# Optimization experiments

Measured on AMD Instinct MI355X. Metric: run time of the kernel, lower is better.

Reference implementation:

```python
import jax, jax.numpy as jnp
import numpy as np

B, T, NX, NY, E, BS = 2, 8, 32, 32, 768, 64
NB = E // BS            # 12 blocks
YM = NY // 2 + 1        # 17 rfft y modes
KM = 12                 # kept_modes (hardcoded in source)
XS = slice(YM - KM, YM + KM)  # slice(5,29) on the x-mode axis (faithful quirk: bounds use y_modes)
LAM = 0.01


def _ln(x, g, b, eps=1e-5):
    m = x.mean(-1, keepdims=True)
    v = ((x - m) ** 2).mean(-1, keepdims=True)
    return (x - m) / jnp.sqrt(v + eps) * g + b


def _softshrink(x, lam=LAM):
    return jnp.where(x > lam, x - lam, jnp.where(x < -lam, x + lam, jnp.zeros((), x.dtype)))


def setup_inputs() -> dict:
    key = jax.random.key(0)
    ks = jax.random.split(key, 8)
    s = 0.02
    return {
        'input': jax.random.normal(ks[0], (B, T, NX * NY, E), jnp.float32),
        'w1': s * jax.random.normal(ks[1], (2, NB, BS, BS), jnp.float32),
        'b1': s * jax.random.normal(ks[2], (2, 1, 1, 1, NB, BS), jnp.float32),
        'w2': s * jax.random.normal(ks[3], (2, NB, BS, BS), jnp.float32),
        'b2': s * jax.random.normal(ks[4], (2, 1, 1, 1, NB, BS), jnp.float32),
        'ln1_g': jnp.ones((E,), jnp.float32),
        'ln1_b': jnp.zeros((E,), jnp.float32),
        'ln2_g': jnp.ones((E,), jnp.float32),
        'ln2_b': jnp.zeros((E,), jnp.float32),
        'mw1': s * jax.random.normal(ks[5], (E, 4 * E), jnp.float32),
        'mb1': jnp.zeros((4 * E,), jnp.float32),
        'mw2': s * jax.random.normal(ks[6], (4 * E, E), jnp.float32),
        'mb2': jnp.zeros((E,), jnp.float32),
    }


def reference(input, w1, b1, w2, b2, ln1_g, ln1_b, ln2_g, ln2_b, mw1, mb1, mw2, mb2):
    residual = input
    h = _ln(input, ln1_g, ln1_b)                       # ln1
    r = h.reshape(B, T, NX, NY, E)
    fc = jnp.fft.rfft2(r, axes=(2, 3), norm='ortho')   # (B,T,NX,YM,E) complex
    fc = fc.reshape(B, T, NX, YM, NB, BS)
    fr = fc.real[:, :, XS, :KM]                        # (B,T,24,12,NB,BS)
    fi = fc.imag[:, :, XS, :KM]
    op = 'btxyni,nio->btxyno'
    o1r = jax.nn.gelu(jnp.einsum(op, fr, w1[0]) - jnp.einsum(op, fi, w1[1]) + b1[0], approximate=False)
    o1i = jax.nn.gelu(jnp.einsum(op, fi, w1[0]) + jnp.einsum(op, fr, w1[1]) + b1[1], approximate=False)
    o2r = jnp.einsum(op, o1r, w2[0]) - jnp.einsum(op, o1i, w2[1]) + b2[0]
    o2i = jnp.einsum(op, o1i, w2[0]) + jnp.einsum(op, o1r, w2[1]) + b2[1]
    out_r = jnp.zeros(fc.shape, jnp.float32).at[:, :, XS, :KM].set(_softshrink(o2r))
    out_i = jnp.zeros(fc.shape, jnp.float32).at[:, :, XS, :KM].set(_softshrink(o2i))
    oc = (out_r + 1j * out_i).reshape(B, T, NX, YM, E)
    spat = jnp.fft.irfft2(oc, s=(NX, NY), axes=(2, 3), norm='ortho').reshape(B, T, NX * NY, E)
    out = spat + h + residual                          # faithful: adds ln1(input) and original input
    res2 = out
    out = _ln(out, ln2_g, ln2_b)                       # ln2
    out = jax.nn.gelu(out @ mw1 + mb1, approximate=False) @ mw2 + mb2
    return out + res2
```

## Files before the change

### kernel.cpp

```cpp
#include <hip/hip_runtime.h>
#include <hip/hip_bf16.h>
#include <math.h>

typedef __bf16 bf16;
typedef __bf16 bf16x8 __attribute__((ext_vector_type(8)));
typedef float f32x4 __attribute__((ext_vector_type(4)));
typedef short short8 __attribute__((ext_vector_type(8)));

#define E_ 768
#define S_ 1024
#define BT_ 16
#define KM_ 12
#define KX_ 24
#define NPOS_ 4608
#define NB_ 12

__device__ __forceinline__ float gelu_exact(float x) {
    return 0.5f * x * (1.0f + erff(x * 0.70710678118654752f));
}

__device__ __forceinline__ bf16x8 neg8(bf16x8 v) {
    short8 s;
    __builtin_memcpy(&s, &v, 16);
    s ^= (short)0x8000;
    bf16x8 r;
    __builtin_memcpy(&r, &s, 16);
    return r;
}

__device__ __forceinline__ void gload16(bf16* lds, const bf16* g) {
    __builtin_amdgcn_global_load_lds(
        (const __attribute__((address_space(1))) void*)g,
        (__attribute__((address_space(3))) void*)lds,
        16, 0, 0);
}

__global__ __launch_bounds__(256) void k_ln_stats(const float* __restrict__ x,
                                                  float* __restrict__ mu, float* __restrict__ rs) {
    int row = blockIdx.x;
    int t = threadIdx.x;
    const float* xr = x + (size_t)row * E_;
    float v0 = xr[t], v1 = xr[t + 256], v2 = xr[t + 512];
    float s = v0 + v1 + v2;
    float ss = v0 * v0 + v1 * v1 + v2 * v2;
    for (int off = 32; off > 0; off >>= 1) {
        s  += __shfl_xor(s, off);
        ss += __shfl_xor(ss, off);
    }
    __shared__ float ls[4], lss[4];
    int w = t >> 6, l = t & 63;
    if (l == 0) { ls[w] = s; lss[w] = ss; }
    __syncthreads();
    if (t == 0) {
        s  = ls[0] + ls[1] + ls[2] + ls[3];
        ss = lss[0] + lss[1] + lss[2] + lss[3];
        float m = s * (1.0f / E_);
        float var = ss * (1.0f / E_) - m * m;
        mu[row] = m;
        rs[row] = rsqrtf(var + 1e-5f);
    }
}

__global__ __launch_bounds__(256) void k_ln2(const float* __restrict__ x,
                                             const float* __restrict__ g,
                                             const float* __restrict__ b,
                                             bf16* __restrict__ out) {
    int row = blockIdx.x;
    int t = threadIdx.x;
    const float* xr = x + (size_t)row * E_;
    float v0 = xr[t], v1 = xr[t + 256], v2 = xr[t + 512];
    float s = v0 + v1 + v2;
    float ss = v0 * v0 + v1 * v1 + v2 * v2;
    for (int off = 32; off > 0; off >>= 1) {
        s  += __shfl_xor(s, off);
        ss += __shfl_xor(ss, off);
    }
    __shared__ float ls[4], lss[4];
    int w = t >> 6, l = t & 63;
    if (l == 0) { ls[w] = s; lss[w] = ss; }
    __syncthreads();
    s  = ls[0] + ls[1] + ls[2] + ls[3];
    ss = lss[0] + lss[1] + lss[2] + lss[3];
    float m = s * (1.0f / E_);
    float var = ss * (1.0f / E_) - m * m;
    float r = rsqrtf(var + 1e-5f);
    #pragma unroll
    for (int q = 0; q < 3; q++) {
        int e = t + q * 256;
        float v = (q == 0) ? v0 : ((q == 1) ? v1 : v2);
        out[(size_t)row * E_ + e] = (bf16)((v - m) * r * g[e] + b[e]);
    }
}

__global__ __launch_bounds__(256) void k_dft_y(const float* __restrict__ inp,
                                               const float* __restrict__ mu, const float* __restrict__ rs,
                                               const float* __restrict__ g, const float* __restrict__ bb,
                                               float* __restrict__ gre, float* __restrict__ gim) {
    int bid = blockIdx.x;
    int ec = bid % 3, x = (bid / 3) % 32, bt = bid / 96;
    int t = threadIdx.x;
    __shared__ float tile[32 * 256];
    __shared__ float c32[32], s32[32];
    if (t < 32) { float a = 6.28318530717958647692f * t / 32.0f; c32[t] = cosf(a); s32[t] = sinf(a); }
    int e = ec * 256 + t;
    float gv = g[e], bv = bb[e];
    int row0 = bt * S_ + x * 32;
    const float* base = inp + (size_t)row0 * E_ + e;
    for (int y = 0; y < 32; y++) {
        float m = mu[row0 + y], r = rs[row0 + y];
        tile[y * 256 + t] = (base[(size_t)y * E_] - m) * r * gv + bv;
    }
    __syncthreads();
    for (int ky = 0; ky < KM_; ky++) {
        float re = 0.f, im = 0.f;
        for (int y = 0; y < 32; y++) {
            int j = (ky * y) & 31;
            float v = tile[y * 256 + t];
            re += v * c32[j];
            im -= v * s32[j];
        }
        size_t o = ((size_t)((bt * 32 + x) * KM_ + ky)) * E_ + e;
        gre[o] = re; gim[o] = im;
    }
}

__global__ __launch_bounds__(256) void k_dft_x(const float* __restrict__ gre, const float* __restrict__ gim,
                                               float* __restrict__ fr, float* __restrict__ fi) {
    int bid = blockIdx.x;
    int ec = bid % 3, ky = (bid / 3) % KM_, bt = bid / (3 * KM_);
    int t = threadIdx.x;
    __shared__ float lre[16 * 256];
    __shared__ float lim[16 * 256];
    __shared__ float c32[32], s32[32];
    if (t < 32) { float a = 6.28318530717958647692f * t / 32.0f; c32[t] = cosf(a); s32[t] = sinf(a); }
    float ar[KX_], ai[KX_];
    #pragma unroll
    for (int k = 0; k < KX_; k++) { ar[k] = 0.f; ai[k] = 0.f; }
    for (int half = 0; half < 2; half++) {
        __syncthreads();
        for (int xi = 0; xi < 16; xi++) {
            int x = half * 16 + xi;
            size_t o = ((size_t)((bt * 32 + x) * KM_ + ky)) * E_ + ec * 256 + t;
            lre[xi * 256 + t] = gre[o];
            lim[xi * 256 + t] = gim[o];
        }
        __syncthreads();
        for (int kxi = 0; kxi < KX_; kxi++) {
            int kx = kxi + 5;
            float re = 0.f, im = 0.f;
            #pragma unroll
            for (int xi = 0; xi < 16; xi++) {
                int j = (kx * (half * 16 + xi)) & 31;
                float c = c32[j], s = s32[j];
                float gr = lre[xi * 256 + t], gi = lim[xi * 256 + t];
                re += gr * c + gi * s;
                im += gi * c - gr * s;
            }
            ar[kxi] += re; ai[kxi] += im;
        }
    }
    #pragma unroll
    for (int kxi = 0; kxi < KX_; kxi++) {
        size_t p = (size_t)(bt * KX_ + kxi) * KM_ + ky;
        fr[p * E_ + ec * 256 + t] = ar[kxi] * (1.0f / 32.0f);
        fi[p * E_ + ec * 256 + t] = ai[kxi] * (1.0f / 32.0f);
    }
}

__global__ __launch_bounds__(256) void k_blockmlp(float* fr, float* fi,
                                                  const float* __restrict__ w1, const float* __restrict__ b1,
                                                  const float* __restrict__ w2, const float* __restrict__ b2) {
    int n = blockIdx.x / 36;
    int p0 = (blockIdx.x % 36) * 128;
    int t = threadIdx.x;
    __shared__ __align__(16) bf16 lXr[128 * 72];
    __shared__ __align__(16) bf16 lXi[128 * 72];
    __shared__ __align__(16) bf16 lW1a[64 * 72];
    __shared__ __align__(16) bf16 lW1b[64 * 72];
    __shared__ __align__(16) bf16 lW2a[64 * 72];
    __shared__ __align__(16) bf16 lW2b[64 * 72];

    {
        int o = t & 63, iq = t >> 6;
        const float* s1a = w1 + (size_t)n * 4096;
        const float* s1b = w1 + (size_t)(NB_ + n) * 4096;
        const float* s2a = w2 + (size_t)n * 4096;
        const float* s2b = w2 + (size_t)(NB_ + n) * 4096;
        #pragma unroll
        for (int ii = 0; ii < 16; ii++) {
            int i = iq * 16 + ii;
            lW1a[o * 72 + i] = (bf16)s1a[i * 64 + o];
            lW1b[o * 72 + i] = (bf16)s1b[i * 64 + o];
            lW2a[o * 72 + i] = (bf16)s2a[i * 64 + o];
            lW2b[o * 72 + i] = (bf16)s2b[i * 64 + o];
        }
    }
    {
        int ch4 = (t & 15) * 4, prow = t >> 4;
        #pragma unroll
        for (int rep = 0; rep < 8; rep++) {
            int p = rep * 16 + prow;
            size_t ga = (size_t)(p0 + p) * E_ + n * 64 + ch4;
            float4 vr = *(const float4*)&fr[ga];
            float4 vi = *(const float4*)&fi[ga];
            bf16 br[4] = {(bf16)vr.x, (bf16)vr.y, (bf16)vr.z, (bf16)vr.w};
            bf16 bi[4] = {(bf16)vi.x, (bf16)vi.y, (bf16)vi.z, (bf16)vi.w};
            *(uint2*)&lXr[p * 72 + ch4] = *(uint2*)br;
            *(uint2*)&lXi[p * 72 + ch4] = *(uint2*)bi;
        }
    }
    int w = t >> 6, l = t & 63, lr = l & 15, lq = l >> 4;
    float bias1r[4], bias1i[4], bias2r[4], bias2i[4];
    #pragma unroll
    for (int ni = 0; ni < 4; ni++) {
        int o = n * 64 + ni * 16 + lr;
        bias1r[ni] = b1[o]; bias1i[ni] = b1[NB_ * 64 + o];
        bias2r[ni] = b2[o]; bias2i[ni] = b2[NB_ * 64 + o];
    }
    __syncthreads();

    f32x4 a1r[2][4], a1i[2][4];
    #pragma unroll
    for (int mt = 0; mt < 2; mt++)
        #pragma unroll
        for (int ni = 0; ni < 4; ni++) { a1r[mt][ni] = (f32x4){0,0,0,0}; a1i[mt][ni] = (f32x4){0,0,0,0}; }
    #pragma unroll
    for (int ks = 0; ks < 2; ks++) {
        int k0 = ks * 32;
        bf16x8 xr[2], xi[2], xin[2];
        #pragma unroll
        for (int mt = 0; mt < 2; mt++) {
            int row = w * 32 + mt * 16 + lr;
            xr[mt]  = *(bf16x8*)&lXr[row * 72 + k0 + lq * 8];
            xi[mt]  = *(bf16x8*)&lXi[row * 72 + k0 + lq * 8];
            xin[mt] = neg8(xi[mt]);
        }
        #pragma unroll
        for (int ni = 0; ni < 4; ni++) {
            bf16x8 ba = *(bf16x8*)&lW1a[(ni * 16 + lr) * 72 + k0 + lq * 8];
            bf16x8 bb = *(bf16x8*)&lW1b[(ni * 16 + lr) * 72 + k0 + lq * 8];
            #pragma unroll
            for (int mt = 0; mt < 2; mt++) {
                a1r[mt][ni] = __builtin_amdgcn_mfma_f32_16x16x32_bf16(xr[mt],  ba, a1r[mt][ni], 0, 0, 0);
                a1r[mt][ni] = __builtin_amdgcn_mfma_f32_16x16x32_bf16(xin[mt], bb, a1r[mt][ni], 0, 0, 0);
                a1i[mt][ni] = __builtin_amdgcn_mfma_f32_16x16x32_bf16(xi[mt],  ba, a1i[mt][ni], 0, 0, 0);
                a1i[mt][ni] = __builtin_amdgcn_mfma_f32_16x16x32_bf16(xr[mt],  bb, a1i[mt][ni], 0, 0, 0);
            }
        }
    }
    #pragma unroll
    for (int mt = 0; mt < 2; mt++)
        #pragma unroll
        for (int ni = 0; ni < 4; ni++) {
            int o = ni * 16 + lr;
            #pragma unroll
            for (int r = 0; r < 4; r++) {
                int row = w * 32 + mt * 16 + lq * 4 + r;
                lXr[row * 72 + o] = (bf16)gelu_exact(a1r[mt][ni][r] + bias1r[ni]);
                lXi[row * 72 + o] = (bf16)gelu_exact(a1i[mt][ni][r] + bias1i[ni]);
            }
        }

    f32x4 a2r[2][4], a2i[2][4];
    #pragma unroll
    for (int mt = 0; mt < 2; mt++)
        #pragma unroll
        for (int ni = 0; ni < 4; ni++) { a2r[mt][ni] = (f32x4){0,0,0,0}; a2i[mt][ni] = (f32x4){0,0,0,0}; }
    #pragma unroll
    for (int ks = 0; ks < 2; ks++) {
        int k0 = ks * 32;
        bf16x8 xr[2], xi[2], xin[2];
        #pragma unroll
        for (int mt = 0; mt < 2; mt++) {
            int row = w * 32 + mt * 16 + lr;
            xr[mt]  = *(bf16x8*)&lXr[row * 72 + k0 + lq * 8];
            xi[mt]  = *(bf16x8*)&lXi[row * 72 + k0 + lq * 8];
            xin[mt] = neg8(xi[mt]);
        }
        #pragma unroll
        for (int ni = 0; ni < 4; ni++) {
            bf16x8 ba = *(bf16x8*)&lW2a[(ni * 16 + lr) * 72 + k0 + lq * 8];
            bf16x8 bb = *(bf16x8*)&lW2b[(ni * 16 + lr) * 72 + k0 + lq * 8];
            #pragma unroll
            for (int mt = 0; mt < 2; mt++) {
                a2r[mt][ni] = __builtin_amdgcn_mfma_f32_16x16x32_bf16(xr[mt],  ba, a2r[mt][ni], 0, 0, 0);
                a2r[mt][ni] = __builtin_amdgcn_mfma_f32_16x16x32_bf16(xin[mt], bb, a2r[mt][ni], 0, 0, 0);
                a2i[mt][ni] = __builtin_amdgcn_mfma_f32_16x16x32_bf16(xi[mt],  ba, a2i[mt][ni], 0, 0, 0);
                a2i[mt][ni] = __builtin_amdgcn_mfma_f32_16x16x32_bf16(xr[mt],  bb, a2i[mt][ni], 0, 0, 0);
            }
        }
    }
    #pragma unroll
    for (int mt = 0; mt < 2; mt++)
        #pragma unroll
        for (int ni = 0; ni < 4; ni++) {
            int o = ni * 16 + lr;
            #pragma unroll
            for (int r = 0; r < 4; r++) {
                int row = w * 32 + mt * 16 + lq * 4 + r;
                float vr = a2r[mt][ni][r] + bias2r[ni];
                float vi = a2i[mt][ni][r] + bias2i[ni];
                vr = (vr > 0.01f) ? vr - 0.01f : ((vr < -0.01f) ? vr + 0.01f : 0.0f);
                vi = (vi > 0.01f) ? vi - 0.01f : ((vi < -0.01f) ? vi + 0.01f : 0.0f);
                size_t ga = (size_t)(p0 + row) * E_ + n * 64 + o;
                fr[ga] = vr;
                fi[ga] = vi;
            }
        }
}

__global__ __launch_bounds__(256) void k_idft_x(const float* __restrict__ pr_, const float* __restrict__ pi_,
                                                float* __restrict__ zre, float* __restrict__ zim) {
    int bid = blockIdx.x;
    int ec = bid % 3, ky = (bid / 3) % KM_, bt = bid / (3 * KM_);
    int t = threadIdx.x;
    __shared__ float lre[KX_ * 256], lim[KX_ * 256];
    __shared__ float c32[32], s32[32];
    if (t < 32) { float a = 6.28318530717958647692f * t / 32.0f; c32[t] = cosf(a); s32[t] = sinf(a); }
    for (int kxi = 0; kxi < KX_; kxi++) {
        size_t p = (size_t)(bt * KX_ + kxi) * KM_ + ky;
        lre[kxi * 256 + t] = pr_[p * E_ + ec * 256 + t];
        lim[kxi * 256 + t] = pi_[p * E_ + ec * 256 + t];
    }
    __syncthreads();
    for (int x = 0; x < 32; x++) {
        float re = 0.f, im = 0.f;
        for (int kxi = 0; kxi < KX_; kxi++) {
            int kx = kxi + 5;
            int j = (kx * x) & 31;
            float c = c32[j], s = s32[j];
            float pr = lre[kxi * 256 + t], pi = lim[kxi * 256 + t];
            re += pr * c - pi * s;
            im += pr * s + pi * c;
        }
        size_t zo = ((size_t)((bt * 32 + x) * KM_ + ky)) * E_ + ec * 256 + t;
        zre[zo] = re; zim[zo] = im;
    }
}

__global__ __launch_bounds__(256) void k_idft_y_res(const float* __restrict__ zre, const float* __restrict__ zim,
                                                    const float* __restrict__ inp,
                                                    const float* __restrict__ mu, const float* __restrict__ rs,
                                                    const float* __restrict__ g, const float* __restrict__ bb,
                                                    float* __restrict__ out) {
    int bid = blockIdx.x;
    int ec = bid % 3, x = (bid / 3) % 32, bt = bid / 96;
    int t = threadIdx.x;
    __shared__ float lre[KM_ * 256], lim[KM_ * 256];
    __shared__ float c32[32], s32[32];
    if (t < 32) { float a = 6.28318530717958647692f * t / 32.0f; c32[t] = cosf(a); s32[t] = sinf(a); }
    for (int ky = 0; ky < KM_; ky++) {
        size_t zo = ((size_t)((bt * 32 + x) * KM_ + ky)) * E_ + ec * 256 + t;
        lre[ky * 256 + t] = zre[zo];
        lim[ky * 256 + t] = zim[zo];
    }
    __syncthreads();
    int e = ec * 256 + t;
    float gv = g[e], bv = bb[e];
    int row0 = bt * S_ + x * 32;
    for (int y = 0; y < 32; y++) {
        float v = lre[t];
        for (int ky = 1; ky < KM_; ky++) {
            int j = (ky * y) & 31;
            v += 2.0f * (lre[ky * 256 + t] * c32[j] - lim[ky * 256 + t] * s32[j]);
        }
        v *= (1.0f / 32.0f);
        size_t o = (size_t)(row0 + y) * E_ + e;
        float iv = inp[o];
        float m = mu[row0 + y], r = rs[row0 + y];
        out[o] = v + ((iv - m) * r * gv + bv) + iv;
    }
}

__global__ void k_transpose_cast(const float* __restrict__ src, bf16* __restrict__ dst, int R, int C) {
    __shared__ float tile[32][33];
    int c0 = blockIdx.x * 32, r0 = blockIdx.y * 32;
    int tx = threadIdx.x, ty = threadIdx.y;
    #pragma unroll
    for (int j = 0; j < 32; j += 8)
        tile[ty + j][tx] = src[(size_t)(r0 + ty + j) * C + c0 + tx];
    __syncthreads();
    #pragma unroll
    for (int j = 0; j < 32; j += 8)
        dst[(size_t)(c0 + ty + j) * R + r0 + tx] = (bf16)tile[tx][ty + j];
}

template<bool FUSE_GELU>
__global__ __launch_bounds__(256) void k_gemm(const bf16* __restrict__ A, const bf16* __restrict__ Bt,
                                              const float* __restrict__ bias, int M, int N, int K,
                                              bf16* __restrict__ outb, float* __restrict__ outf) {
    __shared__ __align__(16) bf16 lA[128 * 32];
    __shared__ __align__(16) bf16 lB[128 * 32];
    int t = threadIdx.x;
    int m0 = blockIdx.x * 128, n0 = blockIdx.y * 128;
    int w = t >> 6, l = t & 63;
    int wm = (w & 1) * 64, wn = (w >> 1) * 64;
    int lr = l & 15, lq = l >> 4;
    f32x4 acc[4][4];
    #pragma unroll
    for (int i = 0; i < 4; i++)
        #pragma unroll
        for (int j = 0; j < 4; j++)
            acc[i][j] = (f32x4){0.f, 0.f, 0.f, 0.f};

    int srow = l >> 2;
    int scol = (l & 3) * 8;
    const bf16* gA0 = A  + (size_t)(m0 + w * 16 + srow) * K + scol;
    const bf16* gA1 = gA0 + (size_t)64 * K;
    const bf16* gB0 = Bt + (size_t)(n0 + w * 16 + srow) * K + scol;
    const bf16* gB1 = gB0 + (size_t)64 * K;
    bf16* sA0 = lA + (w * 16) * 32;
    bf16* sA1 = lA + (64 + w * 16) * 32;
    bf16* sB0 = lB + (w * 16) * 32;
    bf16* sB1 = lB + (64 + w * 16) * 32;

    int nk = K / 32;
    for (int kt = 0; kt < nk; kt++) {
        int ko = kt * 32;
        gload16(sA0, gA0 + ko);
        gload16(sA1, gA1 + ko);
        gload16(sB0, gB0 + ko);
        gload16(sB1, gB1 + ko);
        __syncthreads();
        bf16x8 af[4], bfv[4];
        #pragma unroll
        for (int mi = 0; mi < 4; mi++) af[mi]  = *(bf16x8*)&lA[(wm + mi * 16 + lr) * 32 + lq * 8];
        #pragma unroll
        for (int ni = 0; ni < 4; ni++) bfv[ni] = *(bf16x8*)&lB[(wn + ni * 16 + lr) * 32 + lq * 8];
        #pragma unroll
        for (int mi = 0; mi < 4; mi++)
            #pragma unroll
            for (int ni = 0; ni < 4; ni++)
                acc[mi][ni] = __builtin_amdgcn_mfma_f32_16x16x32_bf16(af[mi], bfv[ni], acc[mi][ni], 0, 0, 0);
        __syncthreads();
    }
    #pragma unroll
    for (int mi = 0; mi < 4; mi++) {
        #pragma unroll
        for (int ni = 0; ni < 4; ni++) {
            int col = n0 + wn + ni * 16 + lr;
            float bv = bias[col];
            #pragma unroll
            for (int r = 0; r < 4; r++) {
                int row = m0 + wm + mi * 16 + lq * 4 + r;
                float v = acc[mi][ni][r] + bv;
                if (FUSE_GELU) {
                    outb[(size_t)row * N + col] = (bf16)gelu_exact(v);
                } else {
                    size_t oo = (size_t)row * N + col;
                    outf[oo] = v + outf[oo];
                }
            }
        }
    }
}

extern "C" void kernel_launch(void* const* d_in, const int* in_sizes, int n_in,
                              void* d_out, int out_size, void* d_ws, size_t ws_size,
                              hipStream_t stream) {
    const float* input = (const float*)d_in[0];
    const float* w1    = (const float*)d_in[1];
    const float* b1    = (const float*)d_in[2];
    const float* w2    = (const float*)d_in[3];
    const float* b2    = (const float*)d_in[4];
    const float* ln1g  = (const float*)d_in[5];
    const float* ln1b  = (const float*)d_in[6];
    const float* ln2g  = (const float*)d_in[7];
    const float* ln2b  = (const float*)d_in[8];
    const float* mw1   = (const float*)d_in[9];
    const float* mb1   = (const float*)d_in[10];
    const float* mw2   = (const float*)d_in[11];
    const float* mb2   = (const float*)d_in[12];
    float* out = (float*)d_out;

    float* ws = (float*)d_ws;
    float* mu  = ws;
    float* rs  = ws + 16384;
    const size_t BASE = 32768;
    float* gre = ws + BASE;
    float* gim = gre + 4718592;
    float* fr  = ws + BASE + 2 * 4718592;
    float* fi  = fr + 3538944;
    bf16* lnA = (bf16*)(ws + BASE);
    bf16* w1T = (bf16*)(ws + BASE + 6291456);
    bf16* w2T = (bf16*)(ws + BASE + 7471104);
    bf16* mid = (bf16*)(ws + BASE + 8650752);

    const size_t fixed_fl = BASE + 6291456 + 1179648 + 1179648;
    size_t avail_fl = ws_size / 4;
    int nch;
    if      (avail_fl >= fixed_fl + 25165824) nch = 1;
    else if (avail_fl >= fixed_fl + 12582912) nch = 2;
    else                                      nch = 4;
    int MC = 16384 / nch;

    k_ln_stats<<<16384, 256, 0, stream>>>(input, mu, rs);
    k_dft_y<<<BT_ * 32 * 3, 256, 0, stream>>>(input, mu, rs, ln1g, ln1b, gre, gim);
    k_dft_x<<<BT_ * KM_ * 3, 256, 0, stream>>>(gre, gim, fr, fi);
    k_blockmlp<<<NB_ * 36, 256, 0, stream>>>(fr, fi, w1, b1, w2, b2);
    k_idft_x<<<BT_ * KM_ * 3, 256, 0, stream>>>(fr, fi, gre, gim);
    k_idft_y_res<<<BT_ * 32 * 3, 256, 0, stream>>>(gre, gim, input, mu, rs, ln1g, ln1b, out);
    k_ln2<<<16384, 256, 0, stream>>>(out, ln2g, ln2b, lnA);
    k_transpose_cast<<<dim3(3072 / 32, 768 / 32), dim3(32, 8), 0, stream>>>(mw1, w1T, 768, 3072);
    k_transpose_cast<<<dim3(768 / 32, 3072 / 32), dim3(32, 8), 0, stream>>>(mw2, w2T, 3072, 768);
    for (int c = 0; c < nch; c++) {
        const bf16* aC = lnA + (size_t)c * MC * 768;
        float* oC = out + (size_t)c * MC * 768;
        k_gemm<true><<<dim3(MC / 128, 24), 256, 0, stream>>>(aC, w1T, mb1, MC, 3072, 768, mid, nullptr);
        k_gemm<false><<<dim3(MC / 128, 6), 256, 0, stream>>>(mid, w2T, mb2, MC, 768, 3072, nullptr, oC);
    }
}
```

Before: 567.5 us.

## Triple-buffer MLP GEMM with 256x256 tiles, swizzled LDS, and async prefetch

The MLP GEMM kernel is rewritten with 256x256 output tiles over 512 threads, so each wave computes 128x64 and more data is reused per LDS load. It adds a three-stage LDS ring with direct global-to-LDS loads issued two tiles ahead, synchronised by vmcnt waits and one barrier per k-step instead of two. An XOR swizzle is applied to the LDS column slots to reduce bank conflicts, and s_setprio raises wave priority around the MFMA block. The costs are higher register pressure from 32 accumulators per wave, 96KB of LDS per block, and fewer blocks for the N=768 GEMM, which may hurt occupancy and tail balance.

```diff
diff --git a/kernel.cpp b/kernel.cpp
--- a/kernel.cpp
+++ b/kernel.cpp
@@ -386,56 +386,79 @@
 }
 
 template<bool FUSE_GELU>
-__global__ __launch_bounds__(256) void k_gemm(const bf16* __restrict__ A, const bf16* __restrict__ Bt,
-                                              const float* __restrict__ bias, int M, int N, int K,
-                                              bf16* __restrict__ outb, float* __restrict__ outf) {
-    __shared__ __align__(16) bf16 lA[128 * 32];
-    __shared__ __align__(16) bf16 lB[128 * 32];
-    int t = threadIdx.x;
-    int m0 = blockIdx.x * 128, n0 = blockIdx.y * 128;
+__global__ __launch_bounds__(512, 2) void k_gemm(const bf16* __restrict__ A, const bf16* __restrict__ Bt,
+                                                 const float* __restrict__ bias, int M, int N, int K,
+                                                 bf16* __restrict__ outb, float* __restrict__ outf) {
+    __shared__ __align__(16) bf16 lA[3][256 * 32];
+    __shared__ __align__(16) bf16 lB[3][256 * 32];
+    int t = threadIdx.x;
+    int m0 = blockIdx.x * 256, n0 = blockIdx.y * 256;
     int w = t >> 6, l = t & 63;
-    int wm = (w & 1) * 64, wn = (w >> 1) * 64;
+    int wm = (w >> 2) * 128, wn = (w & 3) * 64;
     int lr = l & 15, lq = l >> 4;
-    f32x4 acc[4][4];
-    #pragma unroll
-    for (int i = 0; i < 4; i++)
+    int sw = (lr & 3) ^ ((lr >> 2) & 3);
+    int rslot = (lq ^ sw) * 8;
+
+    int rr = l >> 2;
+    int ssw = (rr & 3) ^ ((rr >> 2) & 3);
+    int gcol = ((l & 3) ^ ssw) * 8;
+    const bf16* pA0 = A  + (size_t)(m0 + w * 16 + rr) * K + gcol;
+    const bf16* pA1 = pA0 + (size_t)128 * K;
+    const bf16* pB0 = Bt + (size_t)(n0 + w * 16 + rr) * K + gcol;
+    const bf16* pB1 = pB0 + (size_t)128 * K;
+    int lof0 = (w * 16) * 32;
+    int lof1 = (128 + w * 16) * 32;
+
+    f32x4 acc[8][4];
+    #pragma unroll
+    for (int i = 0; i < 8; i++)
         #pragma unroll
         for (int j = 0; j < 4; j++)
             acc[i][j] = (f32x4){0.f, 0.f, 0.f, 0.f};
 
-    int srow = l >> 2;
-    int scol = (l & 3) * 8;
-    const bf16* gA0 = A  + (size_t)(m0 + w * 16 + srow) * K + scol;
-    const bf16* gA1 = gA0 + (size_t)64 * K;
-    const bf16* gB0 = Bt + (size_t)(n0 + w * 16 + srow) * K + scol;
-    const bf16* gB1 = gB0 + (size_t)64 * K;
-    bf16* sA0 = lA + (w * 16) * 32;
-    bf16* sA1 = lA + (64 + w * 16) * 32;
-    bf16* sB0 = lB + (w * 16) * 32;
-    bf16* sB1 = lB + (64 + w * 16) * 32;
-
     int nk = K / 32;
+#define STAGE(tile, b) do { int _ko = (tile) * 32;          \
+        gload16(&lA[b][lof0], pA0 + _ko);                   \
+        gload16(&lA[b][lof1], pA1 + _ko);                   \
+        gload16(&lB[b][lof0], pB0 + _ko);                   \
+        gload16(&lB[b][lof1], pB1 + _ko); } while (0)
+
+    STAGE(0, 0);
+    STAGE(1, 1);
+    asm volatile("s_waitcnt vmcnt(4)" ::: "memory");
+    __builtin_amdgcn_s_barrier();
+    __builtin_amdgcn_sched_barrier(0);
+
+    int c = 0, cs = 2;
     for (int kt = 0; kt < nk; kt++) {
-        int ko = kt * 32;
-        gload16(sA0, gA0 + ko);
-        gload16(sA1, gA1 + ko);
-        gload16(sB0, gB0 + ko);
-        gload16(sB1, gB1 + ko);
-        __syncthreads();
-        bf16x8 af[4], bfv[4];
-        #pragma unroll
-        for (int mi = 0; mi < 4; mi++) af[mi]  = *(bf16x8*)&lA[(wm + mi * 16 + lr) * 32 + lq * 8];
-        #pragma unroll
-        for (int ni = 0; ni < 4; ni++) bfv[ni] = *(bf16x8*)&lB[(wn + ni * 16 + lr) * 32 + lq * 8];
-        #pragma unroll
-        for (int mi = 0; mi < 4; mi++)
+        if (kt + 2 < nk) STAGE(kt + 2, cs);
+        bf16x8 af[8], bfv[4];
+        #pragma unroll
+        for (int mi = 0; mi < 8; mi++)
+            af[mi] = *(bf16x8*)&lA[c][(wm + mi * 16 + lr) * 32 + rslot];
+        #pragma unroll
+        for (int ni = 0; ni < 4; ni++)
+            bfv[ni] = *(bf16x8*)&lB[c][(wn + ni * 16 + lr) * 32 + rslot];
+        __builtin_amdgcn_s_setprio(1);
+        #pragma unroll
+        for (int mi = 0; mi < 8; mi++)
             #pragma unroll
             for (int ni = 0; ni < 4; ni++)
                 acc[mi][ni] = __builtin_amdgcn_mfma_f32_16x16x32_bf16(af[mi], bfv[ni], acc[mi][ni], 0, 0, 0);
-        __syncthreads();
-    }
-    #pragma unroll
-    for (int mi = 0; mi < 4; mi++) {
+        __builtin_amdgcn_s_setprio(0);
+        if (kt + 1 < nk) {
+            if (kt + 2 < nk) asm volatile("s_waitcnt vmcnt(4)" ::: "memory");
+            else             asm volatile("s_waitcnt vmcnt(0)" ::: "memory");
+            __builtin_amdgcn_s_barrier();
+            __builtin_amdgcn_sched_barrier(0);
+        }
+        c  = (c  == 2) ? 0 : c  + 1;
+        cs = (cs == 2) ? 0 : cs + 1;
+    }
+#undef STAGE
+
+    #pragma unroll
+    for (int mi = 0; mi < 8; mi++) {
         #pragma unroll
         for (int ni = 0; ni < 4; ni++) {
             int col = n0 + wn + ni * 16 + lr;
@@ -506,7 +529,7 @@
     for (int c = 0; c < nch; c++) {
         const bf16* aC = lnA + (size_t)c * MC * 768;
         float* oC = out + (size_t)c * MC * 768;
-        k_gemm<true><<<dim3(MC / 128, 24), 256, 0, stream>>>(aC, w1T, mb1, MC, 3072, 768, mid, nullptr);
-        k_gemm<false><<<dim3(MC / 128, 6), 256, 0, stream>>>(mid, w2T, mb2, MC, 768, 3072, nullptr, oC);
-    }
-}
+        k_gemm<true><<<dim3(MC / 256, 12), 512, 0, stream>>>(aC, w1T, mb1, MC, 3072, 768, mid, nullptr);
+        k_gemm<false><<<dim3(MC / 256, 3), 512, 0, stream>>>(mid, w2T, mb2, MC, 768, 3072, nullptr, oC);
+    }
+}
```

New measurement: 734.6 us. 29.5% more time.

## Double-buffer GEMM LDS tiles and swizzle layout to avoid bank conflicts

Applied to the files above, without the earlier changes.

The MLP GEMM kernel now keeps two LDS buffers and issues the global-to-LDS loads for the next K tile before computing on the current one. This drops one barrier per iteration and overlaps load latency with MFMA work. It also XOR-swizzles the 8-element column slot per row, on both the global source side and the LDS read side, to reduce LDS bank conflicts. The cost is doubled LDS use per block, which may lower occupancy, and correctness depends on gload16 completing before the barrier.

```diff
diff --git a/kernel.cpp b/kernel.cpp
--- a/kernel.cpp
+++ b/kernel.cpp
@@ -389,13 +389,26 @@
 __global__ __launch_bounds__(256) void k_gemm(const bf16* __restrict__ A, const bf16* __restrict__ Bt,
                                               const float* __restrict__ bias, int M, int N, int K,
                                               bf16* __restrict__ outb, float* __restrict__ outf) {
-    __shared__ __align__(16) bf16 lA[128 * 32];
-    __shared__ __align__(16) bf16 lB[128 * 32];
+    __shared__ __align__(16) bf16 lA[2][128 * 32];
+    __shared__ __align__(16) bf16 lB[2][128 * 32];
     int t = threadIdx.x;
     int m0 = blockIdx.x * 128, n0 = blockIdx.y * 128;
     int w = t >> 6, l = t & 63;
     int wm = (w & 1) * 64, wn = (w >> 1) * 64;
     int lr = l & 15, lq = l >> 4;
+    int sw = (lr & 3) ^ ((lr >> 2) & 3);
+    int rslot = (lq ^ sw) * 8;
+
+    int rr = l >> 2;
+    int ssw = (rr & 3) ^ ((rr >> 2) & 3);
+    int gcol = ((l & 3) ^ ssw) * 8;
+    const bf16* pA0 = A  + (size_t)(m0 + w * 16 + rr) * K + gcol;
+    const bf16* pA1 = pA0 + (size_t)64 * K;
+    const bf16* pB0 = Bt + (size_t)(n0 + w * 16 + rr) * K + gcol;
+    const bf16* pB1 = pB0 + (size_t)64 * K;
+    int lof0 = (w * 16) * 32;
+    int lof1 = (64 + w * 16) * 32;
+
     f32x4 acc[4][4];
     #pragma unroll
     for (int i = 0; i < 4; i++)
@@ -403,37 +416,36 @@
         for (int j = 0; j < 4; j++)
             acc[i][j] = (f32x4){0.f, 0.f, 0.f, 0.f};
 
-    int srow = l >> 2;
-    int scol = (l & 3) * 8;
-    const bf16* gA0 = A  + (size_t)(m0 + w * 16 + srow) * K + scol;
-    const bf16* gA1 = gA0 + (size_t)64 * K;
-    const bf16* gB0 = Bt + (size_t)(n0 + w * 16 + srow) * K + scol;
-    const bf16* gB1 = gB0 + (size_t)64 * K;
-    bf16* sA0 = lA + (w * 16) * 32;
-    bf16* sA1 = lA + (64 + w * 16) * 32;
-    bf16* sB0 = lB + (w * 16) * 32;
-    bf16* sB1 = lB + (64 + w * 16) * 32;
-
     int nk = K / 32;
+#define STAGE(tile, b) do { int _ko = (tile) * 32;          \
+        gload16(&lA[b][lof0], pA0 + _ko);                   \
+        gload16(&lA[b][lof1], pA1 + _ko);                   \
+        gload16(&lB[b][lof0], pB0 + _ko);                   \
+        gload16(&lB[b][lof1], pB1 + _ko); } while (0)
+
+    STAGE(0, 0);
+    __syncthreads();
+
+    int cur = 0;
     for (int kt = 0; kt < nk; kt++) {
-        int ko = kt * 32;
-        gload16(sA0, gA0 + ko);
-        gload16(sA1, gA1 + ko);
-        gload16(sB0, gB0 + ko);
-        gload16(sB1, gB1 + ko);
-        __syncthreads();
+        if (kt + 1 < nk) STAGE(kt + 1, cur ^ 1);
         bf16x8 af[4], bfv[4];
         #pragma unroll
-        for (int mi = 0; mi < 4; mi++) af[mi]  = *(bf16x8*)&lA[(wm + mi * 16 + lr) * 32 + lq * 8];
-        #pragma unroll
-        for (int ni = 0; ni < 4; ni++) bfv[ni] = *(bf16x8*)&lB[(wn + ni * 16 + lr) * 32 + lq * 8];
+        for (int mi = 0; mi < 4; mi++)
+            af[mi] = *(bf16x8*)&lA[cur][(wm + mi * 16 + lr) * 32 + rslot];
+        #pragma unroll
+        for (int ni = 0; ni < 4; ni++)
+            bfv[ni] = *(bf16x8*)&lB[cur][(wn + ni * 16 + lr) * 32 + rslot];
         #pragma unroll
         for (int mi = 0; mi < 4; mi++)
             #pragma unroll
             for (int ni = 0; ni < 4; ni++)
                 acc[mi][ni] = __builtin_amdgcn_mfma_f32_16x16x32_bf16(af[mi], bfv[ni], acc[mi][ni], 0, 0, 0);
         __syncthreads();
-    }
+        cur ^= 1;
+    }
+#undef STAGE
+
     #pragma unroll
     for (int mi = 0; mi < 4; mi++) {
         #pragma unroll
```

Result: faster. 534.8 us (-5.8%).
